# Kernel tuning notes

Hardware: AMD Instinct MI355X
Metric: run time of the kernel (lower is better)

Reference implementation:

```python
import jax, jax.numpy as jnp
import numpy as np

TEMPERATURE = 0.5
EPS = 1e-8  # torch.nn.CosineSimilarity eps


def _l2norm(x):
    # torch cosine sim divides by max(||x||, eps) per vector
    n = jnp.sqrt(jnp.sum(x * x, axis=-1, keepdims=True))
    return x / jnp.maximum(n, EPS)


def setup_inputs() -> dict:
    key = jax.random.key(0)
    ka, kb = jax.random.split(key)
    batch_a = jax.random.normal(ka, (4096, 512), dtype=jnp.float32)
    batch_b = jax.random.normal(kb, (4096, 512), dtype=jnp.float32)
    return {"batch_a": batch_a, "batch_b": batch_b}


def reference(batch_a, batch_b):
    a = _l2norm(batch_a)  # [N, D]
    b = _l2norm(batch_b)
    inv_t = 1.0 / TEMPERATURE
    # cosine similarity via normalize + GEMM (same math as broadcast mul+reduce)
    sim11 = (a @ a.T) * inv_t  # [N, N]
    sim22 = (b @ b.T) * inv_t
    sim12 = (a @ b.T) * inv_t
    n = sim12.shape[-1]
    eye = jnp.eye(n, dtype=bool)
    neg_inf = jnp.float32(-jnp.inf)
    sim11 = jnp.where(eye, neg_inf, sim11)
    sim22 = jnp.where(eye, neg_inf, sim22)
    # logits: [[sim12, sim11], [sim22, sim12^T]] -> [2N, 2N]
    logits = jnp.concatenate(
        [jnp.concatenate([sim12, sim11], axis=-1),
         jnp.concatenate([sim22, sim12.T], axis=-1)],
        axis=-2,
    )
    targets = jnp.arange(2 * n)
    logp = jax.nn.log_softmax(logits, axis=-1)  # stable single pass
    loss = -jnp.mean(logp[jnp.arange(2 * n), targets])
    return loss
```

## Files before the change

kernel.cpp:

```cpp
#include <hip/hip_runtime.h>

#define NR 4096
#define DD 512
#define TWO_N 8192
#define MT 64
#define NTILES 2080
#define CHUNK 260

using bf16x8 = __attribute__((ext_vector_type(8))) short;
using f32x4  = __attribute__((ext_vector_type(4))) float;

__device__ __forceinline__ unsigned short f2bf(float f) {
    union { float f; unsigned u; } v; v.f = f;
    unsigned r = v.u + 0x7fff + ((v.u >> 16) & 1);
    return (unsigned short)(r >> 16);
}

__global__ __launch_bounds__(256) void ntx_nrm_kernel(const float* __restrict__ A,
                                                      const float* __restrict__ B,
                                                      unsigned short* __restrict__ X,
                                                      float* __restrict__ d12,
                                                      float* __restrict__ S) {
    const int row = blockIdx.x;
    const int t = threadIdx.x;
    const int lane = t & 63, wid = t >> 6;

    if (t < 2) S[row * 2 + t] = 0.f;

    const float2 av = *(const float2*)(A + row * DD + 2 * t);
    const float2 bv = *(const float2*)(B + row * DD + 2 * t);
    float sa = av.x * av.x + av.y * av.y;
    float sb = bv.x * bv.x + bv.y * bv.y;
#pragma unroll
    for (int o = 32; o; o >>= 1) { sa += __shfl_down(sa, o); sb += __shfl_down(sb, o); }

    __shared__ float red[12];
    if (lane == 0) { red[wid] = sa; red[4 + wid] = sb; }
    __syncthreads();
    const float ta = red[0] + red[1] + red[2] + red[3];
    const float tb = red[4] + red[5] + red[6] + red[7];
    const float ra = 1.f / fmaxf(sqrtf(ta), 1e-8f);
    const float rb = 1.f / fmaxf(sqrtf(tb), 1e-8f);
    const float nax = av.x * ra, nay = av.y * ra;
    const float nbx = bv.x * rb, nby = bv.y * rb;

    *(unsigned*)(X + row * DD + 2 * t) =
        (unsigned)f2bf(nax) | ((unsigned)f2bf(nay) << 16);
    *(unsigned*)(X + (NR + row) * DD + 2 * t) =
        (unsigned)f2bf(nbx) | ((unsigned)f2bf(nby) << 16);

    float dt = nax * nbx + nay * nby;
#pragma unroll
    for (int o = 32; o; o >>= 1) dt += __shfl_down(dt, o);
    if (lane == 0) red[8 + wid] = dt;
    __syncthreads();
    if (t == 0) d12[row] = red[8] + red[9] + red[10] + red[11];
}

__global__ __launch_bounds__(256) void ntx_gemm_lse_kernel(const unsigned short* __restrict__ X,
                                                           float* __restrict__ S) {
    const int bid = blockIdx.x;
    const int sid = (bid & 7) * CHUNK + (bid >> 3);
    int u, v;
    if (sid < 1792) {
        const int s = sid >> 6, loc = sid & 63;
        int U = 0;
        while (7 * (U + 1) - (U + 1) * U / 2 <= s) ++U;
        const int V = U + 1 + (s - (7 * U - U * (U - 1) / 2));
        u = U * 8 + (loc >> 3);
        v = V * 8 + (loc & 7);
    } else {
        const int s2 = sid - 1792;
        const int U = s2 / 36, loc = s2 % 36;
        int lu = 0;
        while ((lu + 1) * 8 - (lu + 1) * lu / 2 <= loc) ++lu;
        const int lv = lu + (loc - (lu * 8 - lu * (lu - 1) / 2));
        u = U * 8 + lu;
        v = U * 8 + lv;
    }
    const bool fixedTile = (u == v);
    const int rowTile = u * 128, colTile = (v ^ 32) * 128;

    __shared__ unsigned short As[2][128 * 32];
    __shared__ unsigned short Bs[2][128 * 32];

    const int t = threadIdx.x;
    const int lane = t & 63, wid = t >> 6;
    const int waveRow = wid >> 1, waveCol = wid & 1;
    const int lr = lane & 15, grp = lane >> 4;
    const int ko = grp * 8;

    f32x4 acc[4][4] = {};

    const int sr = lane >> 2;
    const int sc = (lane & 3) * 8;

    auto STAGE = [&](int sel, int kt) {
#pragma unroll
        for (int q = 0; q < 2; ++q) {
            const int r = (wid * 2 + q) * 16 + sr;
            __builtin_amdgcn_global_load_lds(
                (const __attribute__((address_space(1))) unsigned*)(X + (size_t)(rowTile + r) * DD + kt + sc),
                (__attribute__((address_space(3))) unsigned*)&As[sel][r * 32 + sc], 16, 0, 0);
            __builtin_amdgcn_global_load_lds(
                (const __attribute__((address_space(1))) unsigned*)(X + (size_t)((colTile + r) ^ NR) * DD + kt + sc),
                (__attribute__((address_space(3))) unsigned*)&Bs[sel][r * 32 + sc], 16, 0, 0);
        }
    };

    auto COMPUTE = [&](int sel) {
        bf16x8 af[4], bfr[4];
#pragma unroll
        for (int m = 0; m < 4; ++m)
            af[m] = *(const bf16x8*)&As[sel][(waveRow * 64 + m * 16 + lr) * 32 + ko];
#pragma unroll
        for (int n = 0; n < 4; ++n)
            bfr[n] = *(const bf16x8*)&Bs[sel][(waveCol * 64 + n * 16 + lr) * 32 + ko];
#pragma unroll
        for (int m = 0; m < 4; ++m)
#pragma unroll
            for (int n = 0; n < 4; ++n)
                acc[m][n] = __builtin_amdgcn_mfma_f32_16x16x32_bf16(af[m], bfr[n], acc[m][n], 0, 0, 0);
    };

    STAGE(0, 0);
    STAGE(1, 32);
#pragma unroll
    for (int i = 0; i < 16; ++i) {
        const int cur = i & 1;
        if (i < 15) asm volatile("s_waitcnt vmcnt(4)" ::: "memory");
        else        asm volatile("s_waitcnt vmcnt(0)" ::: "memory");
        __builtin_amdgcn_s_barrier();
        COMPUTE(cur);
        if (i < 14) {
            asm volatile("s_waitcnt lgkmcnt(0)" ::: "memory");
            __builtin_amdgcn_s_barrier();
            STAGE(cur, (i + 2) * 32);
        }
    }

#pragma unroll
    for (int m = 0; m < 4; ++m)
#pragma unroll
        for (int n = 0; n < 4; ++n)
#pragma unroll
            for (int reg = 0; reg < 4; ++reg) {
                const int R = rowTile + waveRow * 64 + m * 16 + grp * 4 + reg;
                const int C = colTile + waveCol * 64 + n * 16 + lr;
                const bool masked = fixedTile && (C == (R ^ NR));
                acc[m][n][reg] = masked ? 0.f : __expf(acc[m][n][reg] * 2.0f);
            }

#pragma unroll
    for (int m = 0; m < 4; ++m)
#pragma unroll
        for (int reg = 0; reg < 4; ++reg) {
            float rs = acc[m][0][reg] + acc[m][1][reg] + acc[m][2][reg] + acc[m][3][reg];
            rs += __shfl_xor(rs, 1);
            rs += __shfl_xor(rs, 2);
            rs += __shfl_xor(rs, 4);
            rs += __shfl_xor(rs, 8);
            if (lr == 0) {
                const int R = rowTile + waveRow * 64 + m * 16 + grp * 4 + reg;
                atomicAdd(&S[R], rs);
            }
        }

    if (!fixedTile) {
#pragma unroll
        for (int n = 0; n < 4; ++n) {
            float cs = 0.f;
#pragma unroll
            for (int m = 0; m < 4; ++m)
#pragma unroll
                for (int reg = 0; reg < 4; ++reg)
                    cs += acc[m][n][reg];
            cs += __shfl_xor(cs, 16);
            cs += __shfl_xor(cs, 32);
            if (grp == 0) {
                const int C = colTile + waveCol * 64 + n * 16 + lr;
                atomicAdd(&S[C ^ NR], cs);
            }
        }
    }
}

__global__ __launch_bounds__(256) void ntx_loss_kernel(const float* __restrict__ S,
                                                       const float* __restrict__ d12,
                                                       float* __restrict__ out) {
    const int t = threadIdx.x;
    float a = 0.f;
    for (int r = t; r < TWO_N; r += 256)
        a += __logf(S[r]) - 2.0f * d12[r & (NR - 1)];
    const int lane = t & 63, wid = t >> 6;
#pragma unroll
    for (int o = 32; o; o >>= 1) a += __shfl_down(a, o);
    __shared__ float red[4];
    if (lane == 0) red[wid] = a;
    __syncthreads();
    if (t == 0) out[0] = (red[0] + red[1] + red[2] + red[3]) * (1.f / (float)TWO_N);
}

extern "C" void kernel_launch(void* const* d_in, const int* in_sizes, int n_in,
                              void* d_out, int out_size, void* d_ws, size_t ws_size,
                              hipStream_t stream) {
    const float* A = (const float*)d_in[0];
    const float* B = (const float*)d_in[1];

    unsigned short* X = (unsigned short*)d_ws;
    float* S   = (float*)((char*)d_ws + (size_t)TWO_N * DD * 2);
    float* d12 = (float*)((char*)S + (size_t)TWO_N * 4);

    ntx_nrm_kernel<<<NR, 256, 0, stream>>>(A, B, X, d12, S);

    ntx_gemm_lse_kernel<<<NTILES, 256, 0, stream>>>(X, S);

    ntx_loss_kernel<<<1, 256, 0, stream>>>(S, d12, (float*)d_out);
}
```

Baseline: 87.01 us.

## Use single-wave 64x64 tiles loading directly from global, parallelize final loss

Replaces the 256-thread 128x128 LDS double-buffered GEMM tile with a single-wave 64x64 tile that loads MFMA fragments straight from global memory (via cache), launching four times as many blocks over the symmetric tile schedule. It removes LDS staging and barriers but raises global/L2 traffic per FLOP and doubles atomic reductions into S. The final loss kernel is spread across 32 blocks with an atomic accumulation into a memset-zeroed output.

Result: slower. 163.4 us (+87.8%).

```diff
diff --git a/kernel.cpp b/kernel.cpp
--- a/kernel.cpp
+++ b/kernel.cpp
@@ -3,9 +3,9 @@
 #define NR 4096
 #define DD 512
 #define TWO_N 8192
-#define MT 64
-#define NTILES 2080
-#define CHUNK 260
+#define WT 128
+#define NWT 8256
+#define CHW 1032
 
 using bf16x8 = __attribute__((ext_vector_type(8))) short;
 using f32x4  = __attribute__((ext_vector_type(4))) float;
@@ -57,20 +57,20 @@
     if (t == 0) d12[row] = red[8] + red[9] + red[10] + red[11];
 }
 
-__global__ __launch_bounds__(256) void ntx_gemm_lse_kernel(const unsigned short* __restrict__ X,
-                                                           float* __restrict__ S) {
+__global__ __launch_bounds__(64) void ntx_gemm_lse_kernel(const unsigned short* __restrict__ X,
+                                                          float* __restrict__ S) {
     const int bid = blockIdx.x;
-    const int sid = (bid & 7) * CHUNK + (bid >> 3);
+    const int sid = (bid & 7) * CHW + (bid >> 3);
     int u, v;
-    if (sid < 1792) {
+    if (sid < 7680) {
         const int s = sid >> 6, loc = sid & 63;
         int U = 0;
-        while (7 * (U + 1) - (U + 1) * U / 2 <= s) ++U;
-        const int V = U + 1 + (s - (7 * U - U * (U - 1) / 2));
+        while (15 * (U + 1) - (U + 1) * U / 2 <= s) ++U;
+        const int V = U + 1 + (s - (15 * U - U * (U - 1) / 2));
         u = U * 8 + (loc >> 3);
         v = V * 8 + (loc & 7);
     } else {
-        const int s2 = sid - 1792;
+        const int s2 = sid - 7680;
         const int U = s2 / 36, loc = s2 % 36;
         int lu = 0;
         while ((lu + 1) * 8 - (lu + 1) * lu / 2 <= loc) ++lu;
@@ -79,64 +79,36 @@
         v = U * 8 + lv;
     }
     const bool fixedTile = (u == v);
-    const int rowTile = u * 128, colTile = (v ^ 32) * 128;
+    const int rowTile = u * 64, colTile = (v ^ 64) * 64;
 
-    __shared__ unsigned short As[2][128 * 32];
-    __shared__ unsigned short Bs[2][128 * 32];
+    const int lane = threadIdx.x & 63;
+    const int lr = lane & 15, grp = lane >> 4;
 
-    const int t = threadIdx.x;
-    const int lane = t & 63, wid = t >> 6;
-    const int waveRow = wid >> 1, waveCol = wid & 1;
-    const int lr = lane & 15, grp = lane >> 4;
-    const int ko = grp * 8;
+    const unsigned short* aP[4];
+    const unsigned short* bP[4];
+#pragma unroll
+    for (int m = 0; m < 4; ++m)
+        aP[m] = X + (size_t)(rowTile + m * 16 + lr) * DD + grp * 8;
+#pragma unroll
+    for (int n = 0; n < 4; ++n)
+        bP[n] = X + (size_t)((colTile + n * 16 + lr) ^ NR) * DD + grp * 8;
 
     f32x4 acc[4][4] = {};
 
-    const int sr = lane >> 2;
-    const int sc = (lane & 3) * 8;
-
-    auto STAGE = [&](int sel, int kt) {
-#pragma unroll
-        for (int q = 0; q < 2; ++q) {
-            const int r = (wid * 2 + q) * 16 + sr;
-            __builtin_amdgcn_global_load_lds(
-                (const __attribute__((address_space(1))) unsigned*)(X + (size_t)(rowTile + r) * DD + kt + sc),
-                (__attribute__((address_space(3))) unsigned*)&As[sel][r * 32 + sc], 16, 0, 0);
-            __builtin_amdgcn_global_load_lds(
-                (const __attribute__((address_space(1))) unsigned*)(X + (size_t)((colTile + r) ^ NR) * DD + kt + sc),
-                (__attribute__((address_space(3))) unsigned*)&Bs[sel][r * 32 + sc], 16, 0, 0);
-        }
-    };
-
-    auto COMPUTE = [&](int sel) {
+#pragma unroll 4
+    for (int kt = 0; kt < 16; ++kt) {
         bf16x8 af[4], bfr[4];
 #pragma unroll
         for (int m = 0; m < 4; ++m)
-            af[m] = *(const bf16x8*)&As[sel][(waveRow * 64 + m * 16 + lr) * 32 + ko];
+            af[m] = *(const bf16x8*)(aP[m] + kt * 32);
 #pragma unroll
         for (int n = 0; n < 4; ++n)
-            bfr[n] = *(const bf16x8*)&Bs[sel][(waveCol * 64 + n * 16 + lr) * 32 + ko];
+            bfr[n] = *(const bf16x8*)(bP[n] + kt * 32);
 #pragma unroll
         for (int m = 0; m < 4; ++m)
 #pragma unroll
             for (int n = 0; n < 4; ++n)
                 acc[m][n] = __builtin_amdgcn_mfma_f32_16x16x32_bf16(af[m], bfr[n], acc[m][n], 0, 0, 0);
-    };
-
-    STAGE(0, 0);
-    STAGE(1, 32);
-#pragma unroll
-    for (int i = 0; i < 16; ++i) {
-        const int cur = i & 1;
-        if (i < 15) asm volatile("s_waitcnt vmcnt(4)" ::: "memory");
-        else        asm volatile("s_waitcnt vmcnt(0)" ::: "memory");
-        __builtin_amdgcn_s_barrier();
-        COMPUTE(cur);
-        if (i < 14) {
-            asm volatile("s_waitcnt lgkmcnt(0)" ::: "memory");
-            __builtin_amdgcn_s_barrier();
-            STAGE(cur, (i + 2) * 32);
-        }
     }
 
 #pragma unroll
@@ -145,8 +117,8 @@
         for (int n = 0; n < 4; ++n)
 #pragma unroll
             for (int reg = 0; reg < 4; ++reg) {
-                const int R = rowTile + waveRow * 64 + m * 16 + grp * 4 + reg;
-                const int C = colTile + waveCol * 64 + n * 16 + lr;
+                const int R = rowTile + m * 16 + grp * 4 + reg;
+                const int C = colTile + n * 16 + lr;
                 const bool masked = fixedTile && (C == (R ^ NR));
                 acc[m][n][reg] = masked ? 0.f : __expf(acc[m][n][reg] * 2.0f);
             }
@@ -161,7 +133,7 @@
             rs += __shfl_xor(rs, 4);
             rs += __shfl_xor(rs, 8);
             if (lr == 0) {
-                const int R = rowTile + waveRow * 64 + m * 16 + grp * 4 + reg;
+                const int R = rowTile + m * 16 + grp * 4 + reg;
                 atomicAdd(&S[R], rs);
             }
         }
@@ -178,7 +150,7 @@
             cs += __shfl_xor(cs, 16);
             cs += __shfl_xor(cs, 32);
             if (grp == 0) {
-                const int C = colTile + waveCol * 64 + n * 16 + lr;
+                const int C = colTile + n * 16 + lr;
                 atomicAdd(&S[C ^ NR], cs);
             }
         }
@@ -189,16 +161,15 @@
                                                        const float* __restrict__ d12,
                                                        float* __restrict__ out) {
     const int t = threadIdx.x;
-    float a = 0.f;
-    for (int r = t; r < TWO_N; r += 256)
-        a += __logf(S[r]) - 2.0f * d12[r & (NR - 1)];
+    const int r = blockIdx.x * 256 + t;
+    float a = __logf(S[r]) - 2.0f * d12[r & (NR - 1)];
     const int lane = t & 63, wid = t >> 6;
 #pragma unroll
     for (int o = 32; o; o >>= 1) a += __shfl_down(a, o);
     __shared__ float red[4];
     if (lane == 0) red[wid] = a;
     __syncthreads();
-    if (t == 0) out[0] = (red[0] + red[1] + red[2] + red[3]) * (1.f / (float)TWO_N);
+    if (t == 0) atomicAdd(out, (red[0] + red[1] + red[2] + red[3]) * (1.f / (float)TWO_N));
 }
 
 extern "C" void kernel_launch(void* const* d_in, const int* in_sizes, int n_in,
@@ -211,9 +182,11 @@
     float* S   = (float*)((char*)d_ws + (size_t)TWO_N * DD * 2);
     float* d12 = (float*)((char*)S + (size_t)TWO_N * 4);
 
+    (void)hipMemsetAsync(d_out, 0, sizeof(float), stream);
+
     ntx_nrm_kernel<<<NR, 256, 0, stream>>>(A, B, X, d12, S);
 
-    ntx_gemm_lse_kernel<<<NTILES, 256, 0, stream>>>(X, S);
+    ntx_gemm_lse_kernel<<<NWT, 64, 0, stream>>>(X, S);
 
-    ntx_loss_kernel<<<1, 256, 0, stream>>>(S, d12, (float*)d_out);
+    ntx_loss_kernel<<<TWO_N / 256, 256, 0, stream>>>(S, d12, (float*)d_out);
 }
```
